# Performance work log

Measured on AMD Instinct MI355X. Metric: run time of the kernel, lower is better.

The kernel has to match this reference:

```python
import jax, jax.numpy as jnp
import numpy as np

H = 512
V = 32000
B = 64
S = 64
T = 64
SOS = 0


def setup_inputs() -> dict:
    key = jax.random.key(0)
    ks = jax.random.split(key, 20)
    s = 1.0 / np.sqrt(H)
    return {
        "encoder_outputs": jax.random.normal(ks[0], (B, S, H), jnp.float32),
        "encoder_hidden": jax.random.normal(ks[1], (1, B, H), jnp.float32),
        "target_tensor": jax.random.randint(ks[2], (B, T), 0, V),
        "emb": jax.random.normal(ks[3], (V, H), jnp.float32) * s,
        "Wa": jax.random.normal(ks[4], (H, H), jnp.float32) * s,
        "ba": jnp.zeros((H,), jnp.float32),
        "Ua": jax.random.normal(ks[5], (H, H), jnp.float32) * s,
        "bu": jnp.zeros((H,), jnp.float32),
        "Va": jax.random.normal(ks[6], (1, H), jnp.float32) * s,
        "bv": jnp.zeros((1,), jnp.float32),
        "W_ih": jax.random.normal(ks[7], (3 * H, 2 * H), jnp.float32) * s,
        "W_hh": jax.random.normal(ks[8], (3 * H, H), jnp.float32) * s,
        "b_ih": jnp.zeros((3 * H,), jnp.float32),
        "b_hh": jnp.zeros((3 * H,), jnp.float32),
        "W_out": jax.random.normal(ks[9], (V, H), jnp.float32) * s,
        "b_out": jnp.zeros((V,), jnp.float32),
    }


def reference(encoder_outputs, encoder_hidden, target_tensor, emb, Wa, ba, Ua, bu,
              Va, bv, W_ih, W_hh, b_ih, b_hh, W_out, b_out):
    # Teacher-forced inputs: SOS then target[:, :-1]
    sos = jnp.full((B, 1), SOS, dtype=target_tensor.dtype)
    inputs = jnp.concatenate([sos, target_tensor[:, :-1]], axis=1)  # [B,T]
    emb_seq = emb[inputs]  # [B,T,H]

    # Precompute Ua(keys): invariant across decode steps
    Uk = jnp.einsum('bsh,kh->bsk', encoder_outputs, Ua) + bu  # [B,S,H]
    h0 = encoder_hidden[0]  # [B,H]

    def step(h, x_t):
        # Bahdanau attention: Va * tanh(Wa q + Ua k)
        q = h @ Wa.T + ba                                   # [B,H]
        scores = jnp.tanh(q[:, None, :] + Uk) @ Va[0] + bv[0]  # [B,S]
        w = jax.nn.softmax(scores, axis=-1)                 # [B,S]
        ctx = jnp.einsum('bs,bsh->bh', w, encoder_outputs)  # [B,H]
        # GRU cell (PyTorch gate layout: r, z, n)
        x = jnp.concatenate([x_t, ctx], axis=-1)            # [B,2H]
        gi = x @ W_ih.T + b_ih
        gh = h @ W_hh.T + b_hh
        ir, iz, inn = jnp.split(gi, 3, axis=-1)
        hr, hz, hn = jnp.split(gh, 3, axis=-1)
        r = jax.nn.sigmoid(ir + hr)
        z = jax.nn.sigmoid(iz + hz)
        n = jnp.tanh(inn + r * hn)
        h_new = (1.0 - z) * n + z * h
        logits = h_new @ W_out.T + b_out                    # [B,V]
        return h_new, (logits, w)

    hT, (logits, attn) = jax.lax.scan(step, h0, jnp.swapaxes(emb_seq, 0, 1))
    log_probs = jax.nn.log_softmax(jnp.swapaxes(logits, 0, 1), axis=-1)  # [B,T,V]
    attentions = jnp.swapaxes(attn, 0, 1)                                # [B,T,S]
    return log_probs, hT[None], attentions
```

## Files before the change

kernel.cpp:

```cpp
#include <hip/hip_runtime.h>
#include <math.h>

#define HH 512
#define VV 32000
#define BB 64
#define SS 64
#define TT 64
#define H3 1536

#define WS_GIEMBBF 0LL
#define WS_UKBF    3145728LL
#define WS_ENCBF   4194304LL
#define WS_EMBBF   5242880LL
#define WS_WCATBF  6291456LL
#define WS_WIHC3   6815744LL
#define WS_WIHE    7208960LL
#define WS_UABF    7602176LL
#define WS_WHH3    7733248LL
#define WS_BCAT    8126464LL
#define WS_QBUF    8128512LL
#define WS_QPART   8161280LL
#define WS_CTXBF   8685568LL
#define WS_H32     8701952LL
#define WS_HBF     8767488LL
#define WS_HSALL   8800256LL

#define OUT_HT  ((long long)BB*TT*VV)
#define OUT_ATT (OUT_HT + (long long)BB*HH)

typedef __attribute__((ext_vector_type(8))) short bf16x8;
typedef __attribute__((ext_vector_type(4))) float f32x4;

__device__ inline unsigned short f2b(float x) {
  unsigned u = __builtin_bit_cast(unsigned, x);
  unsigned r = (u + 0x7FFF + ((u >> 16) & 1)) >> 16;
  return (unsigned short)r;
}
__device__ inline float bc(unsigned u) { return __builtin_bit_cast(float, u); }
__device__ inline float b2f(unsigned short h) { return bc(((unsigned)h) << 16); }
__device__ inline float frcp(float x) { return __builtin_amdgcn_rcpf(x); }
__device__ inline float tanh_fast(float x) { return 1.f - 2.f * frcp(__expf(2.f * x) + 1.f); }
__device__ inline float sigm(float x) { return frcp(1.f + __expf(-x)); }

#define GLDS(gp, lp) __builtin_amdgcn_global_load_lds( \
    (const __attribute__((address_space(1))) void*)(gp), \
    (__attribute__((address_space(3))) void*)(lp), 16, 0, 0)

__global__ __launch_bounds__(256) void build_wcat_kernel(const float* __restrict__ Wa,
    const float* __restrict__ Whh, const float* __restrict__ ba,
    const float* __restrict__ bhh, unsigned short* __restrict__ wcatbf,
    float* __restrict__ bcat)
{
  long long i = (long long)blockIdx.x * 256 + threadIdx.x;
  int j = (int)(i >> 9), k = (int)(i & 511);
  float v = (j < HH) ? Wa[(long long)j*HH + k] : Whh[(long long)(j - HH)*HH + k];
  wcatbf[i] = f2b(v);
  if (i < 2048) bcat[i] = (i < HH) ? ba[i] : bhh[i - HH];
}

__global__ __launch_bounds__(256) void build_g3_kernel(const float* __restrict__ Wsrc,
    unsigned short* __restrict__ o, int ld, int ofs)
{
  long long i = (long long)blockIdx.x * 256 + threadIdx.x;
  int rp = (int)(i >> 9), k = (int)(i & 511);
  int j = rp / 3, g = rp - j * 3;
  o[i] = f2b(Wsrc[((long long)(g*512 + j))*ld + ofs + k]);
}

__global__ __launch_bounds__(256) void build_wihe_kernel(const float* __restrict__ W_ih,
    unsigned short* __restrict__ o)
{
  long long i = (long long)blockIdx.x * 256 + threadIdx.x;
  o[i] = f2b(W_ih[(long long)(i >> 9)*1024 + (i & 511)]);
}

__global__ __launch_bounds__(256) void cvt_f2b_kernel(const float* __restrict__ in,
    unsigned short* __restrict__ outp, long long n)
{
  long long i = ((long long)blockIdx.x * 256 + threadIdx.x) * 4;
  if (i >= n) return;
  float4 v = *(const float4*)(in + i);
  ushort4 r = { f2b(v.x), f2b(v.y), f2b(v.z), f2b(v.w) };
  *(ushort4*)(outp + i) = r;
}

__global__ __launch_bounds__(256) void build_embbf_kernel(const float* __restrict__ emb,
    const int* __restrict__ tgt, unsigned short* __restrict__ embbf)
{
  const int m = blockIdx.x, t = m >> 6, b = m & 63;
  const int tk = (t == 0) ? 0 : tgt[b*TT + t - 1];
  const float* src = emb + (long long)tk*HH;
  unsigned short* dst = embbf + (long long)m*HH;
  const int i = threadIdx.x;
  dst[i] = f2b(src[i]);
  dst[i + 256] = f2b(src[i + 256]);
}

__global__ __launch_bounds__(256) void hinit_kernel(const float* __restrict__ eh,
    unsigned short* __restrict__ hbf0, float* __restrict__ h320)
{
  int i = blockIdx.x * 256 + threadIdx.x;
  float v = eh[i];
  hbf0[i] = f2b(v);
  h320[i] = v;
}

template<int OUTBF>
__global__ __launch_bounds__(256) void mfma_nt(const unsigned short* __restrict__ A,
    const unsigned short* __restrict__ Bw, const float* __restrict__ bias,
    void* __restrict__ Cv, long long ldc)
{
  __shared__ unsigned short As[128*32];
  __shared__ unsigned short Bs[128*32];
  const int tid = threadIdx.x;
  const int w = tid >> 6, l = tid & 63;
  const int m0 = blockIdx.y * 128, n0 = blockIdx.x * 128;
  const int wr = w >> 1, wc = w & 1;

  f32x4 acc[4][4];
  #pragma unroll
  for (int i = 0; i < 4; i++)
    #pragma unroll
    for (int j = 0; j < 4; j++) acc[i][j] = (f32x4){0.f, 0.f, 0.f, 0.f};

  const int srow = l >> 2;
  const int scol = (l & 3) * 8;

  for (int k0 = 0; k0 < HH; k0 += 32) {
    __syncthreads();
    #pragma unroll
    for (int q = 0; q < 2; ++q) {
      int r = w*32 + q*16 + srow;
      GLDS(A  + (long long)(m0 + r)*HH + k0 + scol, As + r*32 + scol);
      GLDS(Bw + (long long)(n0 + r)*HH + k0 + scol, Bs + r*32 + scol);
    }
    __syncthreads();

    bf16x8 a[4], b[4];
    #pragma unroll
    for (int mi = 0; mi < 4; mi++)
      a[mi] = *(const bf16x8*)&As[(wr*64 + mi*16 + (l & 15))*32 + (l >> 4)*8];
    #pragma unroll
    for (int ni = 0; ni < 4; ni++)
      b[ni] = *(const bf16x8*)&Bs[(wc*64 + ni*16 + (l & 15))*32 + (l >> 4)*8];
    #pragma unroll
    for (int mi = 0; mi < 4; mi++)
      #pragma unroll
      for (int ni = 0; ni < 4; ni++)
        acc[mi][ni] = __builtin_amdgcn_mfma_f32_16x16x32_bf16(a[mi], b[ni], acc[mi][ni], 0, 0, 0);
  }

  #pragma unroll
  for (int mi = 0; mi < 4; mi++) {
    #pragma unroll
    for (int ni = 0; ni < 4; ni++) {
      int col = n0 + wc*64 + ni*16 + (l & 15);
      float bb = bias[col];
      #pragma unroll
      for (int r2 = 0; r2 < 4; r2++) {
        int row = m0 + wr*64 + mi*16 + (l >> 4)*4 + r2;
        float v = acc[mi][ni][r2] + bb;
        if (OUTBF) ((unsigned short*)Cv)[(long long)row*ldc + col] = f2b(v);
        else       ((float*)Cv)[(long long)row*ldc + col] = v;
      }
    }
  }
}

__global__ __launch_bounds__(256) void qinit_mfma(
    const unsigned short* __restrict__ hbf_r, const unsigned short* __restrict__ wabf,
    float* __restrict__ qbuf)
{
  __shared__ unsigned short As[64*32];
  __shared__ unsigned short Bs[128*32];
  const int tid = threadIdx.x;
  const int w = tid >> 6, l = tid & 63;
  const int n0 = blockIdx.x * 128;
  const int wr = w >> 1, wc = w & 1;

  f32x4 acc[2][4];
  #pragma unroll
  for (int i = 0; i < 2; i++)
    #pragma unroll
    for (int j = 0; j < 4; j++) acc[i][j] = (f32x4){0.f, 0.f, 0.f, 0.f};

  const int ar = tid >> 2;
  const int ac8 = (tid & 3) * 8;

  for (int k0 = 0; k0 < HH; k0 += 32) {
    __syncthreads();
    GLDS(hbf_r + (long long)ar*HH + k0 + ac8, As + ar*32 + ac8);
    #pragma unroll
    for (int q = 0; q < 2; ++q) {
      int r = q*64 + ar;
      GLDS(wabf + (long long)(n0 + r)*HH + k0 + ac8, Bs + r*32 + ac8);
    }
    __syncthreads();

    bf16x8 a[2], b[4];
    #pragma unroll
    for (int mi = 0; mi < 2; mi++)
      a[mi] = *(const bf16x8*)&As[(wr*32 + mi*16 + (l & 15))*32 + (l >> 4)*8];
    #pragma unroll
    for (int ni = 0; ni < 4; ni++)
      b[ni] = *(const bf16x8*)&Bs[(wc*64 + ni*16 + (l & 15))*32 + (l >> 4)*8];
    #pragma unroll
    for (int mi = 0; mi < 2; mi++)
      #pragma unroll
      for (int ni = 0; ni < 4; ni++)
        acc[mi][ni] = __builtin_amdgcn_mfma_f32_16x16x32_bf16(a[mi], b[ni], acc[mi][ni], 0, 0, 0);
  }

  #pragma unroll
  for (int mi = 0; mi < 2; mi++) {
    #pragma unroll
    for (int ni = 0; ni < 4; ni++) {
      int col = n0 + wc*64 + ni*16 + (l & 15);
      #pragma unroll
      for (int r2 = 0; r2 < 4; r2++) {
        int row = wr*32 + mi*16 + (l >> 4)*4 + r2;
        qbuf[(long long)row*512 + col] = acc[mi][ni][r2];
      }
    }
  }
}

__global__ __launch_bounds__(512) void attn_kernel(int t, int first,
    const float* __restrict__ qbuf, const float* __restrict__ qPart,
    const float* __restrict__ bcat, const unsigned short* __restrict__ ukbf,
    const unsigned short* __restrict__ encbf, const float* __restrict__ Va,
    const float* __restrict__ bvp,
    unsigned short* __restrict__ ctxbf, float* __restrict__ attn_out)
{
  const int b = blockIdx.x, tid = threadIdx.x;
  __shared__ float qs2[8][68];
  __shared__ float vsh[8][68];
  __shared__ float sc[SS], sw[SS];

  {
    const int c = tid;
    float q = bcat[c];
    if (first) {
      q += qbuf[(long long)b*512 + c];
    } else {
      #pragma unroll
      for (int i = 0; i < 16; ++i)
        q += qPart[(long long)i*32768 + b*512 + c];
    }
    qs2[c >> 6][c & 63] = q;
    vsh[c >> 6][c & 63] = Va[c];
  }
  __syncthreads();

  {
    const int s = tid >> 3, sub = tid & 7;
    const uint4* up = (const uint4*)(ukbf + ((long long)(b*SS + s))*512 + sub*64);
    const float* qp = &qs2[sub][0];
    const float* vp = &vsh[sub][0];
    float p_ = 0.f;
    #pragma unroll
    for (int i = 0; i < 8; ++i) {
      uint4 uv = up[i];
      int e = i*8;
      p_ = fmaf(vp[e+0], tanh_fast(qp[e+0] + bc(uv.x << 16)), p_);
      p_ = fmaf(vp[e+1], tanh_fast(qp[e+1] + bc(uv.x & 0xffff0000u)), p_);
      p_ = fmaf(vp[e+2], tanh_fast(qp[e+2] + bc(uv.y << 16)), p_);
      p_ = fmaf(vp[e+3], tanh_fast(qp[e+3] + bc(uv.y & 0xffff0000u)), p_);
      p_ = fmaf(vp[e+4], tanh_fast(qp[e+4] + bc(uv.z << 16)), p_);
      p_ = fmaf(vp[e+5], tanh_fast(qp[e+5] + bc(uv.z & 0xffff0000u)), p_);
      p_ = fmaf(vp[e+6], tanh_fast(qp[e+6] + bc(uv.w << 16)), p_);
      p_ = fmaf(vp[e+7], tanh_fast(qp[e+7] + bc(uv.w & 0xffff0000u)), p_);
    }
    p_ += __shfl_xor(p_, 1);
    p_ += __shfl_xor(p_, 2);
    p_ += __shfl_xor(p_, 4);
    if (sub == 0) sc[s] = p_ + bvp[0];
  }
  __syncthreads();

  if (tid < 64) {
    float x = sc[tid], mx = x;
    #pragma unroll
    for (int off = 32; off; off >>= 1) mx = fmaxf(mx, __shfl_xor(mx, off));
    float e = __expf(x - mx), sm = e;
    #pragma unroll
    for (int off = 32; off; off >>= 1) sm += __shfl_xor(sm, off);
    float w_ = e * frcp(sm);
    sw[tid] = w_;
    attn_out[((long long)b*TT + t)*SS + tid] = w_;
  }
  __syncthreads();

  {
    float a = 0.f;
    const unsigned short* ep = encbf + (long long)b*SS*512 + tid;
    #pragma unroll 8
    for (int s = 0; s < SS; ++s)
      a = fmaf(sw[s], b2f(ep[s*512]), a);
    ctxbf[b*512 + tid] = f2b(a);
  }
}

__global__ __launch_bounds__(256) void gates_qgh_mfma(int t, int last,
    const unsigned short* __restrict__ hbf_r, const unsigned short* __restrict__ ctxbf,
    const unsigned short* __restrict__ wihc3bf, const unsigned short* __restrict__ whh3bf,
    const unsigned short* __restrict__ wabf, const float* __restrict__ bcat,
    const unsigned short* __restrict__ giembbf,
    const float* __restrict__ h32_r, float* __restrict__ h32_w,
    unsigned short* __restrict__ hbf_w, unsigned short* __restrict__ hsall,
    float* __restrict__ out_ht, float* __restrict__ qPart)
{
  __shared__ unsigned short As[64*32];
  __shared__ unsigned short Hs[64*32];
  __shared__ unsigned short Bs[96*32];
  __shared__ unsigned short Cs[96*32];
  __shared__ unsigned short Was[512*32];
  __shared__ unsigned short hnewp[64*40];
  __shared__ float gl[64*100];
  __shared__ float hl[64*100];
  const int tid = threadIdx.x;
  const int w = tid >> 6, l = tid & 63;
  const int n0 = blockIdx.x * 96, j0 = blockIdx.x * 32;
  const int wr = w >> 1, wc = w & 1;

  f32x4 accg[2][3], acch[2][3];
  #pragma unroll
  for (int i = 0; i < 2; i++)
    #pragma unroll
    for (int j = 0; j < 3; j++) {
      accg[i][j] = (f32x4){0.f, 0.f, 0.f, 0.f};
      acch[i][j] = (f32x4){0.f, 0.f, 0.f, 0.f};
    }

  for (int k0 = 0; k0 < HH; k0 += 32) {
    __syncthreads();
    #pragma unroll
    for (int q = 0; q < 5; ++q) {
      int idx = tid + q*256;
      if (idx < 256) {
        int r = idx >> 2, c8 = (idx & 3) * 8;
        GLDS(ctxbf + (long long)r*HH + k0 + c8, As + r*32 + c8);
      } else if (idx < 512) {
        int i2 = idx - 256, r = i2 >> 2, c8 = (i2 & 3) * 8;
        GLDS(hbf_r + (long long)r*HH + k0 + c8, Hs + r*32 + c8);
      } else if (idx < 896) {
        int i2 = idx - 512, r = i2 >> 2, c8 = (i2 & 3) * 8;
        GLDS(wihc3bf + (long long)(n0 + r)*HH + k0 + c8, Bs + r*32 + c8);
      } else {
        int i2 = idx - 896, r = i2 >> 2, c8 = (i2 & 3) * 8;
        GLDS(whh3bf + (long long)(n0 + r)*HH + k0 + c8, Cs + r*32 + c8);
      }
    }
    __syncthreads();

    bf16x8 ag[2], ah[2], bg[3], bh[3];
    #pragma unroll
    for (int mi = 0; mi < 2; mi++) {
      ag[mi] = *(const bf16x8*)&As[(wr*32 + mi*16 + (l & 15))*32 + (l >> 4)*8];
      ah[mi] = *(const bf16x8*)&Hs[(wr*32 + mi*16 + (l & 15))*32 + (l >> 4)*8];
    }
    #pragma unroll
    for (int ni = 0; ni < 3; ni++) {
      bg[ni] = *(const bf16x8*)&Bs[(wc*48 + ni*16 + (l & 15))*32 + (l >> 4)*8];
      bh[ni] = *(const bf16x8*)&Cs[(wc*48 + ni*16 + (l & 15))*32 + (l >> 4)*8];
    }
    #pragma unroll
    for (int mi = 0; mi < 2; mi++)
      #pragma unroll
      for (int ni = 0; ni < 3; ni++) {
        accg[mi][ni] = __builtin_amdgcn_mfma_f32_16x16x32_bf16(ag[mi], bg[ni], accg[mi][ni], 0, 0, 0);
        acch[mi][ni] = __builtin_amdgcn_mfma_f32_16x16x32_bf16(ah[mi], bh[ni], acch[mi][ni], 0, 0, 0);
      }
  }

  if (!last) {
    #pragma unroll
    for (int q = 0; q < 8; ++q) {
      int idx = tid + q*256;
      int r = idx >> 2, c8 = (idx & 3) * 8;
      GLDS(wabf + (long long)r*HH + j0 + c8, Was + r*32 + c8);
    }
  }

  #pragma unroll
  for (int mi = 0; mi < 2; mi++)
    #pragma unroll
    for (int ni = 0; ni < 3; ni++) {
      int col = wc*48 + ni*16 + (l & 15);
      #pragma unroll
      for (int r2 = 0; r2 < 4; r2++) {
        int row = wr*32 + mi*16 + (l >> 4)*4 + r2;
        gl[row*100 + col] = accg[mi][ni][r2];
        hl[row*100 + col] = acch[mi][ni][r2];
      }
    }
  __syncthreads();

  for (int i = tid; i < 2048; i += 256) {
    const int b = i >> 5, jj = i & 31, j = j0 + jj;
    float gcr = gl[b*100 + jj*3 + 0];
    float gcz = gl[b*100 + jj*3 + 1];
    float gcn = gl[b*100 + jj*3 + 2];
    float ghr = hl[b*100 + jj*3 + 0] + bcat[512 + j];
    float ghz = hl[b*100 + jj*3 + 1] + bcat[1024 + j];
    float ghn = hl[b*100 + jj*3 + 2] + bcat[1536 + j];
    const long long gb = ((long long)t*BB + b)*H3 + j;
    float gir = b2f(giembbf[gb]);
    float giz = b2f(giembbf[gb + 512]);
    float gin = b2f(giembbf[gb + 1024]);
    float r = sigm(gir + gcr + ghr);
    float z = sigm(giz + gcz + ghz);
    float n = tanh_fast(gin + gcn + r * ghn);
    float hold = h32_r[b*512 + j];
    float hn = (1.f - z) * n + z * hold;
    h32_w[b*512 + j] = hn;
    unsigned short hb = f2b(hn);
    hbf_w[b*512 + j] = hb;
    hsall[((long long)b*TT + t)*512 + j] = hb;
    hnewp[b*40 + jj] = hb;
    if (t == TT - 1) out_ht[b*512 + j] = hn;
  }
  __syncthreads();

  if (!last) {
    f32x4 qa[4][8];
    #pragma unroll
    for (int mi = 0; mi < 4; mi++)
      #pragma unroll
      for (int ni = 0; ni < 8; ni++) qa[mi][ni] = (f32x4){0.f, 0.f, 0.f, 0.f};

    bf16x8 a[4];
    #pragma unroll
    for (int mi = 0; mi < 4; mi++)
      a[mi] = *(const bf16x8*)&hnewp[(mi*16 + (l & 15))*40 + (l >> 4)*8];
    #pragma unroll
    for (int ni = 0; ni < 8; ni++) {
      bf16x8 bfr = *(const bf16x8*)&Was[(w*128 + ni*16 + (l & 15))*32 + (l >> 4)*8];
      #pragma unroll
      for (int mi = 0; mi < 4; mi++)
        qa[mi][ni] = __builtin_amdgcn_mfma_f32_16x16x32_bf16(a[mi], bfr, qa[mi][ni], 0, 0, 0);
    }

    float* qp = qPart + (long long)blockIdx.x * 32768;
    #pragma unroll
    for (int mi = 0; mi < 4; mi++)
      #pragma unroll
      for (int ni = 0; ni < 8; ni++) {
        int col = w*128 + ni*16 + (l & 15);
        #pragma unroll
        for (int r2 = 0; r2 < 4; r2++) {
          int row = mi*16 + (l >> 4)*4 + r2;
          qp[row*512 + col] = qa[mi][ni][r2];
        }
      }
  }
}

__global__ __launch_bounds__(1024) void logsoftmax_kernel(float* __restrict__ lp)
{
  float4* p4 = (float4*)(lp + (long long)blockIdx.x * VV);
  const int tid = threadIdx.x;
  float m = -1e30f, s = 0.f;
  for (int v = tid; v < 8000; v += 1024) {
    float4 x = p4[v];
    float mx = fmaxf(fmaxf(x.x, x.y), fmaxf(x.z, x.w));
    float e = __expf(x.x - mx) + __expf(x.y - mx) + __expf(x.z - mx) + __expf(x.w - mx);
    if (mx > m) { s = s * __expf(m - mx) + e; m = mx; }
    else        { s += e * __expf(mx - m); }
  }
  #pragma unroll
  for (int off = 32; off; off >>= 1) {
    float m2 = __shfl_xor(m, off), s2 = __shfl_xor(s, off);
    float mm = fmaxf(m, m2);
    s = s * __expf(m - mm) + s2 * __expf(m2 - mm);
    m = mm;
  }
  __shared__ float rm[16], rs[16];
  if ((tid & 63) == 0) { rm[tid >> 6] = m; rs[tid >> 6] = s; }
  __syncthreads();
  float M = rm[0], S = rs[0];
  #pragma unroll
  for (int i = 1; i < 16; ++i) {
    float m2 = rm[i], s2 = rs[i];
    float mm = fmaxf(M, m2);
    S = S * __expf(M - mm) + s2 * __expf(m2 - mm);
    M = mm;
  }
  const float L = M + logf(S);
  for (int v = tid; v < 8000; v += 1024) {
    float4 x = p4[v];
    x.x -= L; x.y -= L; x.z -= L; x.w -= L;
    p4[v] = x;
  }
}

extern "C" void kernel_launch(void* const* d_in, const int* in_sizes, int n_in,
                              void* d_out, int out_size, void* d_ws, size_t ws_size,
                              hipStream_t stream)
{
  const float* enc   = (const float*)d_in[0];
  const float* eh    = (const float*)d_in[1];
  const int*   tgt   = (const int*)  d_in[2];
  const float* emb   = (const float*)d_in[3];
  const float* Wa    = (const float*)d_in[4];
  const float* ba    = (const float*)d_in[5];
  const float* Ua    = (const float*)d_in[6];
  const float* bu    = (const float*)d_in[7];
  const float* Va    = (const float*)d_in[8];
  const float* bvp   = (const float*)d_in[9];
  const float* W_ih  = (const float*)d_in[10];
  const float* W_hh  = (const float*)d_in[11];
  const float* b_ih  = (const float*)d_in[12];
  const float* b_hh  = (const float*)d_in[13];
  const float* W_out = (const float*)d_in[14];
  const float* b_out = (const float*)d_in[15];

  float* out = (float*)d_out;
  float* ws  = (float*)d_ws;

  unsigned short* giembbf = (unsigned short*)(ws + WS_GIEMBBF);
  unsigned short* ukbf    = (unsigned short*)(ws + WS_UKBF);
  unsigned short* encbf   = (unsigned short*)(ws + WS_ENCBF);
  unsigned short* embbf   = (unsigned short*)(ws + WS_EMBBF);
  unsigned short* wcatbf  = (unsigned short*)(ws + WS_WCATBF);
  unsigned short* wihc3bf = (unsigned short*)(ws + WS_WIHC3);
  unsigned short* wihebf  = (unsigned short*)(ws + WS_WIHE);
  unsigned short* uabf    = (unsigned short*)(ws + WS_UABF);
  unsigned short* whh3bf  = (unsigned short*)(ws + WS_WHH3);
  float* bcat  = ws + WS_BCAT;
  float* qbuf  = ws + WS_QBUF;
  float* qPart = ws + WS_QPART;
  unsigned short* ctxbf = (unsigned short*)(ws + WS_CTXBF);
  float* h320 = ws + WS_H32;
  float* h321 = h320 + BB*HH;
  unsigned short* hbf0 = (unsigned short*)(ws + WS_HBF);
  unsigned short* hbf1 = hbf0 + BB*HH;
  unsigned short* hsall = (unsigned short*)(ws + WS_HSALL);
  unsigned short* wbf   = (unsigned short*)ws;

  float* attn_out = out + OUT_ATT;
  float* out_ht   = out + OUT_HT;

  build_wcat_kernel<<<dim3(4096), dim3(256), 0, stream>>>(Wa, W_hh, ba, b_hh, wcatbf, bcat);
  build_g3_kernel<<<dim3(3072), dim3(256), 0, stream>>>(W_ih, wihc3bf, 1024, 512);
  build_g3_kernel<<<dim3(3072), dim3(256), 0, stream>>>(W_hh, whh3bf, 512, 0);
  build_wihe_kernel<<<dim3(3072), dim3(256), 0, stream>>>(W_ih, wihebf);
  cvt_f2b_kernel<<<dim3(256), dim3(256), 0, stream>>>(Ua, uabf, (long long)HH*HH);
  cvt_f2b_kernel<<<dim3(2048), dim3(256), 0, stream>>>(enc, encbf, (long long)BB*SS*HH);
  build_embbf_kernel<<<dim3(4096), dim3(256), 0, stream>>>(emb, tgt, embbf);
  hinit_kernel<<<dim3(128), dim3(256), 0, stream>>>(eh, hbf0, h320);

  mfma_nt<1><<<dim3(4, 32), dim3(256), 0, stream>>>(encbf, uabf, bu, (void*)ukbf, (long long)HH);
  mfma_nt<1><<<dim3(12, 32), dim3(256), 0, stream>>>(embbf, wihebf, b_ih, (void*)giembbf, (long long)H3);

  qinit_mfma<<<dim3(4), dim3(256), 0, stream>>>(hbf0, wcatbf, qbuf);

  for (int t = 0; t < TT; ++t) {
    const unsigned short* hr  = (t & 1) ? hbf1 : hbf0;
    const float*          h32r = (t & 1) ? h321 : h320;
    unsigned short*       hw  = (t & 1) ? hbf0 : hbf1;
    float*                h32w = (t & 1) ? h320 : h321;
    attn_kernel<<<dim3(64), dim3(512), 0, stream>>>(t, (t == 0) ? 1 : 0, qbuf, qPart,
        bcat, ukbf, encbf, Va, bvp, ctxbf, attn_out);
    gates_qgh_mfma<<<dim3(16), dim3(256), 0, stream>>>(t, (t == TT - 1) ? 1 : 0,
        hr, ctxbf, wihc3bf, whh3bf, wcatbf, bcat, giembbf,
        h32r, h32w, hw, hsall, out_ht, qPart);
  }

  cvt_f2b_kernel<<<dim3(16000), dim3(256), 0, stream>>>(W_out, wbf, (long long)VV*HH);
  mfma_nt<0><<<dim3(250, 32), dim3(256), 0, stream>>>(hsall, wbf, b_out, (void*)out, (long long)VV);
  logsoftmax_kernel<<<dim3(4096), dim3(1024), 0, stream>>>(out);
}
```

Baseline: 2.183 ms.

## Fuse attention and GRU gate kernels into one launch with flag sync

Merges the per-step attention kernel and the gates/q-projection kernel into a single 80-block launch. The first 64 blocks compute attention and signal an atomic flag, and the remaining 16 blocks spin on that flag before running the GRU GEMMs. The gate blocks now use 512 threads, with half the waves doing the ctx GEMM and half the h GEMM. Log-softmax also keeps its row in registers instead of re-reading it from memory. This cuts launch count per step, but it relies on all 80 blocks being co-resident so the spin-wait cannot deadlock.

Result: slower. 2.314 ms (+6.0%).

```diff
diff --git a/kernel.cpp b/kernel.cpp
--- a/kernel.cpp
+++ b/kernel.cpp
@@ -24,6 +24,7 @@
 #define WS_H32     8701952LL
 #define WS_HBF     8767488LL
 #define WS_HSALL   8800256LL
+#define WS_FLAGS   9848832LL
 
 #define OUT_HT  ((long long)BB*TT*VV)
 #define OUT_ATT (OUT_HT + (long long)BB*HH)
@@ -225,91 +226,22 @@
   }
 }
 
-__global__ __launch_bounds__(512) void attn_kernel(int t, int first,
-    const float* __restrict__ qbuf, const float* __restrict__ qPart,
+__global__ __launch_bounds__(512) void step_fused(int t, int first, int last,
+    const float* __restrict__ qbuf, float* __restrict__ qPart,
     const float* __restrict__ bcat, const unsigned short* __restrict__ ukbf,
     const unsigned short* __restrict__ encbf, const float* __restrict__ Va,
-    const float* __restrict__ bvp,
-    unsigned short* __restrict__ ctxbf, float* __restrict__ attn_out)
-{
-  const int b = blockIdx.x, tid = threadIdx.x;
-  __shared__ float qs2[8][68];
-  __shared__ float vsh[8][68];
-  __shared__ float sc[SS], sw[SS];
-
-  {
-    const int c = tid;
-    float q = bcat[c];
-    if (first) {
-      q += qbuf[(long long)b*512 + c];
-    } else {
-      #pragma unroll
-      for (int i = 0; i < 16; ++i)
-        q += qPart[(long long)i*32768 + b*512 + c];
-    }
-    qs2[c >> 6][c & 63] = q;
-    vsh[c >> 6][c & 63] = Va[c];
-  }
-  __syncthreads();
-
-  {
-    const int s = tid >> 3, sub = tid & 7;
-    const uint4* up = (const uint4*)(ukbf + ((long long)(b*SS + s))*512 + sub*64);
-    const float* qp = &qs2[sub][0];
-    const float* vp = &vsh[sub][0];
-    float p_ = 0.f;
-    #pragma unroll
-    for (int i = 0; i < 8; ++i) {
-      uint4 uv = up[i];
-      int e = i*8;
-      p_ = fmaf(vp[e+0], tanh_fast(qp[e+0] + bc(uv.x << 16)), p_);
-      p_ = fmaf(vp[e+1], tanh_fast(qp[e+1] + bc(uv.x & 0xffff0000u)), p_);
-      p_ = fmaf(vp[e+2], tanh_fast(qp[e+2] + bc(uv.y << 16)), p_);
-      p_ = fmaf(vp[e+3], tanh_fast(qp[e+3] + bc(uv.y & 0xffff0000u)), p_);
-      p_ = fmaf(vp[e+4], tanh_fast(qp[e+4] + bc(uv.z << 16)), p_);
-      p_ = fmaf(vp[e+5], tanh_fast(qp[e+5] + bc(uv.z & 0xffff0000u)), p_);
-      p_ = fmaf(vp[e+6], tanh_fast(qp[e+6] + bc(uv.w << 16)), p_);
-      p_ = fmaf(vp[e+7], tanh_fast(qp[e+7] + bc(uv.w & 0xffff0000u)), p_);
-    }
-    p_ += __shfl_xor(p_, 1);
-    p_ += __shfl_xor(p_, 2);
-    p_ += __shfl_xor(p_, 4);
-    if (sub == 0) sc[s] = p_ + bvp[0];
-  }
-  __syncthreads();
-
-  if (tid < 64) {
-    float x = sc[tid], mx = x;
-    #pragma unroll
-    for (int off = 32; off; off >>= 1) mx = fmaxf(mx, __shfl_xor(mx, off));
-    float e = __expf(x - mx), sm = e;
-    #pragma unroll
-    for (int off = 32; off; off >>= 1) sm += __shfl_xor(sm, off);
-    float w_ = e * frcp(sm);
-    sw[tid] = w_;
-    attn_out[((long long)b*TT + t)*SS + tid] = w_;
-  }
-  __syncthreads();
-
-  {
-    float a = 0.f;
-    const unsigned short* ep = encbf + (long long)b*SS*512 + tid;
-    #pragma unroll 8
-    for (int s = 0; s < SS; ++s)
-      a = fmaf(sw[s], b2f(ep[s*512]), a);
-    ctxbf[b*512 + tid] = f2b(a);
-  }
-}
-
-__global__ __launch_bounds__(256) void gates_qgh_mfma(int t, int last,
-    const unsigned short* __restrict__ hbf_r, const unsigned short* __restrict__ ctxbf,
+    const float* __restrict__ bvp, unsigned short* __restrict__ ctxbf,
+    float* __restrict__ attn_out,
+    const unsigned short* __restrict__ hbf_r,
     const unsigned short* __restrict__ wihc3bf, const unsigned short* __restrict__ whh3bf,
-    const unsigned short* __restrict__ wabf, const float* __restrict__ bcat,
-    const unsigned short* __restrict__ giembbf,
+    const unsigned short* __restrict__ wabf, const unsigned short* __restrict__ giembbf,
     const float* __restrict__ h32_r, float* __restrict__ h32_w,
     unsigned short* __restrict__ hbf_w, unsigned short* __restrict__ hsall,
-    float* __restrict__ out_ht, float* __restrict__ qPart)
-{
+    float* __restrict__ out_ht, int* __restrict__ flags)
+{
+  const int bid = blockIdx.x, tid = threadIdx.x;
+  const int w = tid >> 6, l = tid & 63;
+
   __shared__ unsigned short As[64*32];
   __shared__ unsigned short Hs[64*32];
   __shared__ unsigned short Bs[96*32];
@@ -318,25 +250,104 @@
   __shared__ unsigned short hnewp[64*40];
   __shared__ float gl[64*100];
   __shared__ float hl[64*100];
-  const int tid = threadIdx.x;
-  const int w = tid >> 6, l = tid & 63;
-  const int n0 = blockIdx.x * 96, j0 = blockIdx.x * 32;
-  const int wr = w >> 1, wc = w & 1;
-
-  f32x4 accg[2][3], acch[2][3];
+  __shared__ float qs2[8][68];
+  __shared__ float vsh[8][68];
+  __shared__ float sc[SS], sw[SS];
+
+  if (bid < 64) {
+    const int b = bid;
+    {
+      const int c = tid;
+      float q = bcat[c];
+      if (first) {
+        q += qbuf[(long long)b*512 + c];
+      } else {
+        #pragma unroll
+        for (int i = 0; i < 16; ++i)
+          q += qPart[(long long)i*32768 + b*512 + c];
+      }
+      qs2[c >> 6][c & 63] = q;
+      vsh[c >> 6][c & 63] = Va[c];
+    }
+    __syncthreads();
+
+    {
+      const int s = tid >> 3, sub = tid & 7;
+      const uint4* up = (const uint4*)(ukbf + ((long long)(b*SS + s))*512 + sub*64);
+      const float* qp = &qs2[sub][0];
+      const float* vp = &vsh[sub][0];
+      float p_ = 0.f;
+      #pragma unroll
+      for (int i = 0; i < 8; ++i) {
+        uint4 uv = up[i];
+        int e = i*8;
+        p_ = fmaf(vp[e+0], tanh_fast(qp[e+0] + bc(uv.x << 16)), p_);
+        p_ = fmaf(vp[e+1], tanh_fast(qp[e+1] + bc(uv.x & 0xffff0000u)), p_);
+        p_ = fmaf(vp[e+2], tanh_fast(qp[e+2] + bc(uv.y << 16)), p_);
+        p_ = fmaf(vp[e+3], tanh_fast(qp[e+3] + bc(uv.y & 0xffff0000u)), p_);
+        p_ = fmaf(vp[e+4], tanh_fast(qp[e+4] + bc(uv.z << 16)), p_);
+        p_ = fmaf(vp[e+5], tanh_fast(qp[e+5] + bc(uv.z & 0xffff0000u)), p_);
+        p_ = fmaf(vp[e+6], tanh_fast(qp[e+6] + bc(uv.w << 16)), p_);
+        p_ = fmaf(vp[e+7], tanh_fast(qp[e+7] + bc(uv.w & 0xffff0000u)), p_);
+      }
+      p_ += __shfl_xor(p_, 1);
+      p_ += __shfl_xor(p_, 2);
+      p_ += __shfl_xor(p_, 4);
+      if (sub == 0) sc[s] = p_ + bvp[0];
+    }
+    __syncthreads();
+
+    if (tid < 64) {
+      float x = sc[tid], mx = x;
+      #pragma unroll
+      for (int off = 32; off; off >>= 1) mx = fmaxf(mx, __shfl_xor(mx, off));
+      float e = __expf(x - mx), sm = e;
+      #pragma unroll
+      for (int off = 32; off; off >>= 1) sm += __shfl_xor(sm, off);
+      float w_ = e * frcp(sm);
+      sw[tid] = w_;
+      attn_out[((long long)b*TT + t)*SS + tid] = w_;
+    }
+    __syncthreads();
+
+    {
+      float a = 0.f;
+      const unsigned short* ep = encbf + (long long)b*SS*512 + tid;
+      #pragma unroll 8
+      for (int s = 0; s < SS; ++s)
+        a = fmaf(sw[s], b2f(ep[s*512]), a);
+      ctxbf[b*512 + tid] = f2b(a);
+    }
+    __syncthreads();
+    if (tid == 0)
+      __hip_atomic_fetch_add(&flags[t], 1, __ATOMIC_RELEASE, __HIP_MEMORY_SCOPE_AGENT);
+    return;
+  }
+
+  const int blk = bid - 64;
+  const int n0 = blk * 96, j0 = blk * 32;
+
+  if (tid == 0) {
+    while (__hip_atomic_load(&flags[t], __ATOMIC_ACQUIRE, __HIP_MEMORY_SCOPE_AGENT) < 64)
+      __builtin_amdgcn_s_sleep(2);
+  }
+  __syncthreads();
+  __threadfence();
+
+  const int wl4 = w & 3;
+  const int wr = wl4 >> 1, wc = wl4 & 1;
+
+  f32x4 acc2[2][3];
   #pragma unroll
   for (int i = 0; i < 2; i++)
     #pragma unroll
-    for (int j = 0; j < 3; j++) {
-      accg[i][j] = (f32x4){0.f, 0.f, 0.f, 0.f};
-      acch[i][j] = (f32x4){0.f, 0.f, 0.f, 0.f};
-    }
+    for (int j = 0; j < 3; j++) acc2[i][j] = (f32x4){0.f, 0.f, 0.f, 0.f};
 
   for (int k0 = 0; k0 < HH; k0 += 32) {
     __syncthreads();
     #pragma unroll
-    for (int q = 0; q < 5; ++q) {
-      int idx = tid + q*256;
+    for (int q = 0; q < 3; ++q) {
+      int idx = tid + q*512;
       if (idx < 256) {
         int r = idx >> 2, c8 = (idx & 3) * 8;
         GLDS(ctxbf + (long long)r*HH + k0 + c8, As + r*32 + c8);
@@ -346,57 +357,55 @@
       } else if (idx < 896) {
         int i2 = idx - 512, r = i2 >> 2, c8 = (i2 & 3) * 8;
         GLDS(wihc3bf + (long long)(n0 + r)*HH + k0 + c8, Bs + r*32 + c8);
-      } else {
+      } else if (idx < 1280) {
         int i2 = idx - 896, r = i2 >> 2, c8 = (i2 & 3) * 8;
         GLDS(whh3bf + (long long)(n0 + r)*HH + k0 + c8, Cs + r*32 + c8);
       }
     }
     __syncthreads();
 
-    bf16x8 ag[2], ah[2], bg[3], bh[3];
-    #pragma unroll
-    for (int mi = 0; mi < 2; mi++) {
-      ag[mi] = *(const bf16x8*)&As[(wr*32 + mi*16 + (l & 15))*32 + (l >> 4)*8];
-      ah[mi] = *(const bf16x8*)&Hs[(wr*32 + mi*16 + (l & 15))*32 + (l >> 4)*8];
-    }
-    #pragma unroll
-    for (int ni = 0; ni < 3; ni++) {
-      bg[ni] = *(const bf16x8*)&Bs[(wc*48 + ni*16 + (l & 15))*32 + (l >> 4)*8];
-      bh[ni] = *(const bf16x8*)&Cs[(wc*48 + ni*16 + (l & 15))*32 + (l >> 4)*8];
-    }
+    const unsigned short* Ap = (w < 4) ? As : Hs;
+    const unsigned short* Bp = (w < 4) ? Bs : Cs;
+    bf16x8 a[2], b[3];
     #pragma unroll
     for (int mi = 0; mi < 2; mi++)
-      #pragma unroll
-      for (int ni = 0; ni < 3; ni++) {
-        accg[mi][ni] = __builtin_amdgcn_mfma_f32_16x16x32_bf16(ag[mi], bg[ni], accg[mi][ni], 0, 0, 0);
-        acch[mi][ni] = __builtin_amdgcn_mfma_f32_16x16x32_bf16(ah[mi], bh[ni], acch[mi][ni], 0, 0, 0);
-      }
+      a[mi] = *(const bf16x8*)&Ap[(wr*32 + mi*16 + (l & 15))*32 + (l >> 4)*8];
+    #pragma unroll
+    for (int ni = 0; ni < 3; ni++)
+      b[ni] = *(const bf16x8*)&Bp[(wc*48 + ni*16 + (l & 15))*32 + (l >> 4)*8];
+    #pragma unroll
+    for (int mi = 0; mi < 2; mi++)
+      #pragma unroll
+      for (int ni = 0; ni < 3; ni++)
+        acc2[mi][ni] = __builtin_amdgcn_mfma_f32_16x16x32_bf16(a[mi], b[ni], acc2[mi][ni], 0, 0, 0);
   }
 
   if (!last) {
     #pragma unroll
-    for (int q = 0; q < 8; ++q) {
-      int idx = tid + q*256;
+    for (int q = 0; q < 4; ++q) {
+      int idx = tid + q*512;
       int r = idx >> 2, c8 = (idx & 3) * 8;
       GLDS(wabf + (long long)r*HH + j0 + c8, Was + r*32 + c8);
     }
   }
 
-  #pragma unroll
-  for (int mi = 0; mi < 2; mi++)
-    #pragma unroll
-    for (int ni = 0; ni < 3; ni++) {
-      int col = wc*48 + ni*16 + (l & 15);
-      #pragma unroll
-      for (int r2 = 0; r2 < 4; r2++) {
-        int row = wr*32 + mi*16 + (l >> 4)*4 + r2;
-        gl[row*100 + col] = accg[mi][ni][r2];
-        hl[row*100 + col] = acch[mi][ni][r2];
-      }
-    }
+  {
+    float* dst = (w < 4) ? gl : hl;
+    #pragma unroll
+    for (int mi = 0; mi < 2; mi++)
+      #pragma unroll
+      for (int ni = 0; ni < 3; ni++) {
+        int col = wc*48 + ni*16 + (l & 15);
+        #pragma unroll
+        for (int r2 = 0; r2 < 4; r2++) {
+          int row = wr*32 + mi*16 + (l >> 4)*4 + r2;
+          dst[row*100 + col] = acc2[mi][ni][r2];
+        }
+      }
+  }
   __syncthreads();
 
-  for (int i = tid; i < 2048; i += 256) {
+  for (int i = tid; i < 2048; i += 512) {
     const int b = i >> 5, jj = i & 31, j = j0 + jj;
     float gcr = gl[b*100 + jj*3 + 0];
     float gcz = gl[b*100 + jj*3 + 1];
@@ -423,30 +432,30 @@
   __syncthreads();
 
   if (!last) {
-    f32x4 qa[4][8];
+    f32x4 qa[4][4];
     #pragma unroll
     for (int mi = 0; mi < 4; mi++)
       #pragma unroll
-      for (int ni = 0; ni < 8; ni++) qa[mi][ni] = (f32x4){0.f, 0.f, 0.f, 0.f};
+      for (int ni = 0; ni < 4; ni++) qa[mi][ni] = (f32x4){0.f, 0.f, 0.f, 0.f};
 
     bf16x8 a[4];
     #pragma unroll
     for (int mi = 0; mi < 4; mi++)
       a[mi] = *(const bf16x8*)&hnewp[(mi*16 + (l & 15))*40 + (l >> 4)*8];
     #pragma unroll
-    for (int ni = 0; ni < 8; ni++) {
-      bf16x8 bfr = *(const bf16x8*)&Was[(w*128 + ni*16 + (l & 15))*32 + (l >> 4)*8];
+    for (int ni = 0; ni < 4; ni++) {
+      bf16x8 bfr = *(const bf16x8*)&Was[(w*64 + ni*16 + (l & 15))*32 + (l >> 4)*8];
       #pragma unroll
       for (int mi = 0; mi < 4; mi++)
         qa[mi][ni] = __builtin_amdgcn_mfma_f32_16x16x32_bf16(a[mi], bfr, qa[mi][ni], 0, 0, 0);
     }
 
-    float* qp = qPart + (long long)blockIdx.x * 32768;
+    float* qp = qPart + (long long)blk * 32768;
     #pragma unroll
     for (int mi = 0; mi < 4; mi++)
       #pragma unroll
-      for (int ni = 0; ni < 8; ni++) {
-        int col = w*128 + ni*16 + (l & 15);
+      for (int ni = 0; ni < 4; ni++) {
+        int col = w*64 + ni*16 + (l & 15);
         #pragma unroll
         for (int r2 = 0; r2 < 4; r2++) {
           int row = mi*16 + (l >> 4)*4 + r2;
@@ -460,13 +469,19 @@
 {
   float4* p4 = (float4*)(lp + (long long)blockIdx.x * VV);
   const int tid = threadIdx.x;
+  float4 x[8];
   float m = -1e30f, s = 0.f;
-  for (int v = tid; v < 8000; v += 1024) {
-    float4 x = p4[v];
-    float mx = fmaxf(fmaxf(x.x, x.y), fmaxf(x.z, x.w));
-    float e = __expf(x.x - mx) + __expf(x.y - mx) + __expf(x.z - mx) + __expf(x.w - mx);
-    if (mx > m) { s = s * __expf(m - mx) + e; m = mx; }
-    else        { s += e * __expf(mx - m); }
+  #pragma unroll
+  for (int i = 0; i < 8; ++i) {
+    int v = tid + i*1024;
+    if (v < 8000) {
+      float4 xx = p4[v];
+      x[i] = xx;
+      float mx = fmaxf(fmaxf(xx.x, xx.y), fmaxf(xx.z, xx.w));
+      float e = __expf(xx.x - mx) + __expf(xx.y - mx) + __expf(xx.z - mx) + __expf(xx.w - mx);
+      if (mx > m) { s = s * __expf(m - mx) + e; m = mx; }
+      else        { s += e * __expf(mx - m); }
+    }
   }
   #pragma unroll
   for (int off = 32; off; off >>= 1) {
@@ -487,10 +502,14 @@
     M = mm;
   }
   const float L = M + logf(S);
-  for (int v = tid; v < 8000; v += 1024) {
-    float4 x = p4[v];
-    x.x -= L; x.y -= L; x.z -= L; x.w -= L;
-    p4[v] = x;
+  #pragma unroll
+  for (int i = 0; i < 8; ++i) {
+    int v = tid + i*1024;
+    if (v < 8000) {
+      float4 xx = x[i];
+      xx.x -= L; xx.y -= L; xx.z -= L; xx.w -= L;
+      p4[v] = xx;
+    }
   }
 }
 
@@ -536,11 +555,13 @@
   unsigned short* hbf0 = (unsigned short*)(ws + WS_HBF);
   unsigned short* hbf1 = hbf0 + BB*HH;
   unsigned short* hsall = (unsigned short*)(ws + WS_HSALL);
+  int* flags = (int*)(ws + WS_FLAGS);
   unsigned short* wbf   = (unsigned short*)ws;
 
   float* attn_out = out + OUT_ATT;
   float* out_ht   = out + OUT_HT;
 
+  hipMemsetAsync(flags, 0, TT * sizeof(int), stream);
   build_wcat_kernel<<<dim3(4096), dim3(256), 0, stream>>>(Wa, W_hh, ba, b_hh, wcatbf, bcat);
   build_g3_kernel<<<dim3(3072), dim3(256), 0, stream>>>(W_ih, wihc3bf, 1024, 512);
   build_g3_kernel<<<dim3(3072), dim3(256), 0, stream>>>(W_hh, whh3bf, 512, 0);
@@ -560,11 +581,10 @@
     const float*          h32r = (t & 1) ? h321 : h320;
     unsigned short*       hw  = (t & 1) ? hbf0 : hbf1;
     float*                h32w = (t & 1) ? h320 : h321;
-    attn_kernel<<<dim3(64), dim3(512), 0, stream>>>(t, (t == 0) ? 1 : 0, qbuf, qPart,
-        bcat, ukbf, encbf, Va, bvp, ctxbf, attn_out);
-    gates_qgh_mfma<<<dim3(16), dim3(256), 0, stream>>>(t, (t == TT - 1) ? 1 : 0,
-        hr, ctxbf, wihc3bf, whh3bf, wcatbf, bcat, giembbf,
-        h32r, h32w, hw, hsall, out_ht, qPart);
+    step_fused<<<dim3(80), dim3(512), 0, stream>>>(t, (t == 0) ? 1 : 0,
+        (t == TT - 1) ? 1 : 0, qbuf, qPart, bcat, ukbf, encbf, Va, bvp,
+        ctxbf, attn_out, hr, wihc3bf, whh3bf, wcatbf, giembbf,
+        h32r, h32w, hw, hsall, out_ht, flags);
   }
 
   cvt_f2b_kernel<<<dim3(16000), dim3(256), 0, stream>>>(W_out, wbf, (long long)VV*HH);
```
